# Kernel optimization log

Measured on AMD Instinct MI355X. Metric: run time of the kernel, lower is better.

Reference implementation:

```python
import jax, jax.numpy as jnp
import numpy as np

N, K, D, V = 20000, 16, 256, 64  # nodes, neighbors, embed_dim, edge vocab


def setup_inputs() -> dict:
    key = jax.random.key(0)
    ks = jax.random.split(key, 16)
    s = 1.0 / np.sqrt(2 * D)  # Linear(512 -> 256) init scale
    return {
        "node_reps": jax.random.normal(ks[0], (1, N, D), jnp.float32),
        "in_indices": jax.random.randint(ks[1], (1, N, K), 0, N, jnp.int32),
        "in_edges": jax.random.randint(ks[2], (1, N, K), 0, V, jnp.int32),
        "in_mask": jax.random.uniform(ks[3], (1, N, K), jnp.float32),
        "out_indices": jax.random.randint(ks[4], (1, N, K), 0, N, jnp.int32),
        "out_edges": jax.random.randint(ks[5], (1, N, K), 0, V, jnp.int32),
        "out_mask": jax.random.uniform(ks[6], (1, N, K), jnp.float32),
        "edge_emb_1": jax.random.normal(ks[7], (V, D), jnp.float32),
        "W_1": jax.random.uniform(ks[8], (2 * D, D), jnp.float32, -s, s),
        "b_1": jnp.zeros((D,), jnp.float32),
        "edge_emb_2": jax.random.normal(ks[9], (V, D), jnp.float32),
        "W_2": jax.random.uniform(ks[10], (2 * D, D), jnp.float32, -s, s),
        "b_2": jnp.zeros((D,), jnp.float32),
        "edge_emb_3": jax.random.normal(ks[11], (V, D), jnp.float32),
        "W_3": jax.random.uniform(ks[12], (2 * D, D), jnp.float32, -s, s),
        "b_3": jnp.zeros((D,), jnp.float32),
    }


def gcn_layer(node_reps, in_idx, in_edg, in_msk, out_idx, out_edg, out_msk,
              edge_emb, W, b):
    # node_reps: [1, N, D]; dropout is identity in eval mode.
    nodes = node_reps[0]  # [N, D]; batch_size == 1 as in the original repo

    def agg(idx, edg, msk):
        nbr = nodes[idx]          # gather: [1, N, K, D]
        erep = edge_emb[edg]      # embedding lookup: [1, N, K, D]
        reps = jnp.concatenate([nbr, erep], axis=3) * msk[..., None]
        return reps.sum(axis=2)   # masked sum over neighbors: [1, N, 2D]

    in_reps = agg(in_idx, in_edg, in_msk)
    out_reps = agg(out_idx, out_edg, out_msk)
    in_nodes = in_reps[0] @ W + b    # [N, D]
    out_nodes = out_reps[0] @ W + b  # [N, D]
    return node_reps + out_nodes + in_nodes  # broadcast -> [1, N, D]


def reference(node_reps, in_indices, in_edges, in_mask,
              out_indices, out_edges, out_mask,
              edge_emb_1, W_1, b_1, edge_emb_2, W_2, b_2, edge_emb_3, W_3, b_3):
    nbrs = (in_indices, in_edges, in_mask, out_indices, out_edges, out_mask)
    hidden = gcn_layer(node_reps, *nbrs, edge_emb_1, W_1, b_1)  # gc1
    mu = gcn_layer(hidden, *nbrs, edge_emb_2, W_2, b_2)          # gc2
    logvar = gcn_layer(hidden, *nbrs, edge_emb_3, W_3, b_3)      # gc3

    mu_t = jnp.tanh(mu[0])        # [N, D]
    lv_t = jnp.tanh(logvar[0])    # [N, D]
    n_nodes = mu_t.shape[0]
    kld = (-0.5 / n_nodes) * jnp.mean(
        jnp.sum(1.0 + 2.0 * lv_t - mu_t ** 2 - jnp.exp(lv_t) ** 2, axis=1))
    return hidden, kld
```

## Files before the change

### kernel.cpp

```cpp
#include <hip/hip_runtime.h>
#include <math.h>

#define NN 20000
#define KK 16
#define DD 256
#define VV 64
#define NT1 16
#define NT23 32

typedef __attribute__((ext_vector_type(8))) __bf16 bf16x8;
typedef __attribute__((ext_vector_type(4))) float floatx4;
typedef __attribute__((ext_vector_type(2))) float floatx2;
typedef __attribute__((ext_vector_type(8))) unsigned short ushort8;

__device__ __forceinline__ float4 ld4(const float* p) { return *reinterpret_cast<const float4*>(p); }

__device__ __forceinline__ unsigned short f2bf(float f) {
    union { float f; unsigned u; } v; v.f = f;
    unsigned r = v.u + 0x7FFFu + ((v.u >> 16) & 1u);
    return (unsigned short)(r >> 16);
}
__device__ __forceinline__ float bf2f(unsigned short u) {
    union { unsigned u; float f; } v; v.u = ((unsigned)u) << 16;
    return v.f;
}
__device__ __forceinline__ unsigned char f2q(float f) {
    return (unsigned char)(__builtin_amdgcn_cvt_pk_fp8_f32(f, 0.f, 0u, false) & 0xFFu);
}
__device__ __forceinline__ float q2f(unsigned char q) {
    floatx2 r = __builtin_amdgcn_cvt_pk_f32_fp8((unsigned)q, false);
    return r.x;
}

__global__ __launch_bounds__(256) void ewk3(const float* __restrict__ e1, const float* __restrict__ W1,
                                            const float* __restrict__ e2, const float* __restrict__ W2,
                                            const float* __restrict__ e3, const float* __restrict__ W3,
                                            float* __restrict__ EW) {
    int layer = blockIdx.y;
    const float* emb = layer == 0 ? e1 : (layer == 1 ? e2 : e3);
    const float* W   = layer == 0 ? W1 : (layer == 1 ? W2 : W3);
    int v = blockIdx.x, d = threadIdx.x;
    float acc = 0.f;
    #pragma unroll 8
    for (int j = 0; j < 256; ++j)
        acc += emb[v * DD + j] * W[(size_t)(256 + j) * DD + d];
    EW[(size_t)layer * VV * DD + v * DD + d] = acc;
}

__global__ __launch_bounds__(256) void packU2(const float* __restrict__ W1, const float* __restrict__ EW1,
                                              const float* __restrict__ W2, const float* __restrict__ EW2,
                                              const float* __restrict__ W3, const float* __restrict__ EW3,
                                              unsigned short* __restrict__ U1, unsigned short* __restrict__ U23) {
    int blk = blockIdx.x;
    int NT; unsigned short* U; const float *Wa, *EWa, *Wb, *EWb; int g;
    if (blk < 40) { NT = NT1;  U = U1;  Wa = W1; EWa = EW1; Wb = W1; EWb = EW1; g = blk * 256 + threadIdx.x; }
    else          { NT = NT23; U = U23; Wa = W2; EWa = EW2; Wb = W3; EWb = EW3; g = (blk - 40) * 256 + threadIdx.x; }
    int lane = g & 63, ntk = g >> 6;
    int nt = ntk % NT, kt = ntk / NT;
    if (kt >= 10) return;
    int n = nt * 16 + (lane & 15);
    int kbase = kt * 32 + (lane >> 4) * 8;
    const float* W = Wa; const float* EW = EWa;
    if (n >= 256) { W = Wb; EW = EWb; n -= 256; }
    unsigned short o8[8];
    #pragma unroll
    for (int j = 0; j < 8; ++j) {
        int k = kbase + j;
        float v = (k < 256) ? W[(size_t)k * DD + n] : EW[(size_t)(k - 256) * DD + n];
        o8[j] = f2bf(v);
    }
    *reinterpret_cast<uint4*>(&U[(size_t)g * 8]) = *reinterpret_cast<uint4*>(o8);
}

__global__ __launch_bounds__(256) void prep(const int* __restrict__ ie, const float* __restrict__ im,
                                            const int* __restrict__ oe, const float* __restrict__ om,
                                            const float* __restrict__ x,
                                            unsigned short* __restrict__ Sb, unsigned short* __restrict__ xh) {
    int w = threadIdx.x >> 6, lane = threadIdx.x & 63;
    int n = blockIdx.x * 4 + w;
    int e = 0; float m = 0.f;
    if (lane < 16)      { e = ie[n * KK + lane];      m = im[n * KK + lane]; }
    else if (lane < 32) { e = oe[n * KK + lane - 16]; m = om[n * KK + lane - 16]; }
    float h = 0.f;
    #pragma unroll
    for (int j = 0; j < 32; ++j) {
        int ev = __shfl(e, j);
        float mv = __shfl(m, j);
        if (ev == lane) h += mv;
    }
    Sb[(size_t)n * 320 + 256 + lane] = f2bf(h);
    if (xh) {
        size_t base = (size_t)blockIdx.x * 1024 + threadIdx.x * 4;
        float4 v = ld4(x + base);
        ushort4 o; o.x = f2bf(v.x); o.y = f2bf(v.y); o.z = f2bf(v.z); o.w = f2bf(v.w);
        *reinterpret_cast<ushort4*>(xh + base) = o;
    }
}

__global__ __launch_bounds__(256) void aggh(const unsigned short* __restrict__ src, const int* __restrict__ ii,
                                            const float* __restrict__ im, const int* __restrict__ oi,
                                            const float* __restrict__ om, unsigned short* __restrict__ Sb) {
    int w = threadIdx.x >> 6, lane = threadIdx.x & 63;
    int n = blockIdx.x * 4 + w;
    __shared__ int sidx[4][32];
    __shared__ float smsk[4][32];
    if (lane < 16) {
        sidx[w][lane] = ii[n * KK + lane]; sidx[w][lane + 16] = oi[n * KK + lane];
        smsk[w][lane] = im[n * KK + lane]; smsk[w][lane + 16] = om[n * KK + lane];
    }
    __syncthreads();
    int half = lane >> 5, c = (lane & 31) * 8;
    float acc[8] = {0.f, 0.f, 0.f, 0.f, 0.f, 0.f, 0.f, 0.f};
    #pragma unroll
    for (int j = 0; j < 16; ++j) {
        int j2 = j * 2 + half;
        int idx = sidx[w][j2];
        float m = smsk[w][j2];
        ushort8 u = *reinterpret_cast<const ushort8*>(src + (size_t)idx * DD + c);
        #pragma unroll
        for (int z = 0; z < 8; ++z) acc[z] += m * bf2f(u[z]);
    }
    #pragma unroll
    for (int z = 0; z < 8; ++z) acc[z] += __shfl_xor(acc[z], 32);
    if (half == 0) {
        unsigned short o8[8];
        #pragma unroll
        for (int z = 0; z < 8; ++z) o8[z] = f2bf(acc[z]);
        *reinterpret_cast<uint4*>(&Sb[(size_t)n * 320 + c]) = *reinterpret_cast<uint4*>(o8);
    }
}

__global__ __launch_bounds__(256) void aggq(const unsigned char* __restrict__ src, const int* __restrict__ ii,
                                            const float* __restrict__ im, const int* __restrict__ oi,
                                            const float* __restrict__ om, unsigned short* __restrict__ Sb) {
    int w = threadIdx.x >> 6, lane = threadIdx.x & 63;
    int n = blockIdx.x * 4 + w;
    __shared__ int sidx[4][32];
    __shared__ float smsk[4][32];
    if (lane < 16) {
        sidx[w][lane] = ii[n * KK + lane]; sidx[w][lane + 16] = oi[n * KK + lane];
        smsk[w][lane] = im[n * KK + lane]; smsk[w][lane + 16] = om[n * KK + lane];
    }
    __syncthreads();
    int g = lane >> 4, cl = lane & 15;
    float acc[16];
    #pragma unroll
    for (int z = 0; z < 16; ++z) acc[z] = 0.f;
    #pragma unroll
    for (int j = 0; j < 8; ++j) {
        int r = g * 8 + j;
        int idx = sidx[w][r];
        float m = smsk[w][r];
        uint4 u = *reinterpret_cast<const uint4*>(src + (size_t)idx * DD + cl * 16);
        unsigned dw[4] = {u.x, u.y, u.z, u.w};
        #pragma unroll
        for (int d = 0; d < 4; ++d) {
            floatx2 f01 = __builtin_amdgcn_cvt_pk_f32_fp8(dw[d], false);
            floatx2 f23 = __builtin_amdgcn_cvt_pk_f32_fp8(dw[d], true);
            acc[d * 4 + 0] += m * f01.x; acc[d * 4 + 1] += m * f01.y;
            acc[d * 4 + 2] += m * f23.x; acc[d * 4 + 3] += m * f23.y;
        }
    }
    #pragma unroll
    for (int z = 0; z < 16; ++z) {
        acc[z] += __shfl_xor(acc[z], 16);
        acc[z] += __shfl_xor(acc[z], 32);
    }
    if (g == 0) {
        unsigned short o16[16];
        #pragma unroll
        for (int z = 0; z < 16; ++z) o16[z] = f2bf(acc[z]);
        uint4* dst = reinterpret_cast<uint4*>(&Sb[(size_t)n * 320 + cl * 16]);
        dst[0] = reinterpret_cast<uint4*>(o16)[0];
        dst[1] = reinterpret_cast<uint4*>(o16)[1];
    }
}

__global__ __launch_bounds__(256) void aggf(const float* __restrict__ src, const int* __restrict__ ii,
                                            const float* __restrict__ im, const int* __restrict__ oi,
                                            const float* __restrict__ om, unsigned short* __restrict__ Sb) {
    int w = threadIdx.x >> 6, lane = threadIdx.x & 63;
    int n = blockIdx.x * 4 + w;
    __shared__ int sidx[4][32];
    __shared__ float smsk[4][32];
    if (lane < 16) {
        sidx[w][lane] = ii[n * KK + lane]; sidx[w][lane + 16] = oi[n * KK + lane];
        smsk[w][lane] = im[n * KK + lane]; smsk[w][lane + 16] = om[n * KK + lane];
    }
    __syncthreads();
    int c = lane * 4;
    float4 s = make_float4(0.f, 0.f, 0.f, 0.f);
    #pragma unroll 4
    for (int j = 0; j < 32; ++j) {
        float4 xr = ld4(src + (size_t)sidx[w][j] * DD + c);
        float m = smsk[w][j];
        s.x += m * xr.x; s.y += m * xr.y; s.z += m * xr.z; s.w += m * xr.w;
    }
    ushort4 o; o.x = f2bf(s.x); o.y = f2bf(s.y); o.z = f2bf(s.z); o.w = f2bf(s.w);
    *reinterpret_cast<ushort4*>(&Sb[(size_t)n * 320 + c]) = o;
}

__global__ __launch_bounds__(256) void mm1(const unsigned short* __restrict__ Sb, const unsigned short* __restrict__ U,
                                           const float* __restrict__ x, const float* __restrict__ b,
                                           float* __restrict__ out, unsigned char* __restrict__ h8) {
    __shared__ unsigned short sA[16 * 336];
    int n0 = blockIdx.x * 16;
    for (int c = threadIdx.x; c < 640; c += 256) {
        int row = c / 40, k8 = c % 40;
        *reinterpret_cast<uint4*>(&sA[row * 336 + k8 * 8]) =
            *reinterpret_cast<const uint4*>(&Sb[(size_t)(n0 + row) * 320 + k8 * 8]);
    }
    __syncthreads();
    int lane = threadIdx.x & 63, w = threadIdx.x >> 6;
    int lr = lane & 15, quad = lane >> 4;
    float xp[4][4], bb[4];
    #pragma unroll
    for (int t = 0; t < 4; ++t) {
        int col = (w * 4 + t) * 16 + lr;
        bb[t] = 2.f * b[col];
        #pragma unroll
        for (int r = 0; r < 4; ++r)
            xp[t][r] = x[(size_t)(n0 + quad * 4 + r) * DD + col];
    }
    floatx4 z = {0.f, 0.f, 0.f, 0.f};
    floatx4 acc[4] = {z, z, z, z};
    for (int kt = 0; kt < 10; ++kt) {
        bf16x8 a = *reinterpret_cast<const bf16x8*>(&sA[lr * 336 + kt * 32 + quad * 8]);
        #pragma unroll
        for (int t = 0; t < 4; ++t) {
            bf16x8 bf = *reinterpret_cast<const bf16x8*>(&U[(size_t)((kt * NT1 + w * 4 + t) * 64 + lane) * 8]);
            acc[t] = __builtin_amdgcn_mfma_f32_16x16x32_bf16(a, bf, acc[t], 0, 0, 0);
        }
    }
    #pragma unroll
    for (int t = 0; t < 4; ++t) {
        int col = (w * 4 + t) * 16 + lr;
        #pragma unroll
        for (int r = 0; r < 4; ++r) {
            size_t o = (size_t)(n0 + quad * 4 + r) * DD + col;
            float v = xp[t][r] + bb[t] + acc[t][r];
            out[o] = v;
            if (h8) h8[o] = f2q(v);
        }
    }
}

__global__ __launch_bounds__(256) void mm23(const unsigned short* __restrict__ Sb, const unsigned short* __restrict__ U,
                                            const unsigned char* __restrict__ h8, const float* __restrict__ hf,
                                            const float* __restrict__ b2, const float* __restrict__ b3,
                                            float* __restrict__ partials) {
    __shared__ unsigned short sA[16 * 336];
    __shared__ float red[4];
    int n0 = blockIdx.x * 16, pass = blockIdx.y;
    for (int c = threadIdx.x; c < 640; c += 256) {
        int row = c / 40, k8 = c % 40;
        *reinterpret_cast<uint4*>(&sA[row * 336 + k8 * 8]) =
            *reinterpret_cast<const uint4*>(&Sb[(size_t)(n0 + row) * 320 + k8 * 8]);
    }
    __syncthreads();
    int lane = threadIdx.x & 63, w = threadIdx.x >> 6;
    int lr = lane & 15, quad = lane >> 4;
    const float* b = pass ? b3 : b2;
    float hp[4][4], bb[4];
    #pragma unroll
    for (int t = 0; t < 4; ++t) {
        int col = (w * 4 + t) * 16 + lr;
        bb[t] = 2.f * b[col];
        #pragma unroll
        for (int r = 0; r < 4; ++r) {
            size_t o = (size_t)(n0 + quad * 4 + r) * DD + col;
            hp[t][r] = h8 ? q2f(h8[o]) : hf[o];
        }
    }
    floatx4 z = {0.f, 0.f, 0.f, 0.f};
    floatx4 acc[4] = {z, z, z, z};
    for (int kt = 0; kt < 10; ++kt) {
        bf16x8 a = *reinterpret_cast<const bf16x8*>(&sA[lr * 336 + kt * 32 + quad * 8]);
        #pragma unroll
        for (int t = 0; t < 4; ++t) {
            int nt = pass * 16 + w * 4 + t;
            bf16x8 bf = *reinterpret_cast<const bf16x8*>(&U[(size_t)((kt * NT23 + nt) * 64 + lane) * 8]);
            acc[t] = __builtin_amdgcn_mfma_f32_16x16x32_bf16(a, bf, acc[t], 0, 0, 0);
        }
    }
    float kacc = 0.f;
    #pragma unroll
    for (int t = 0; t < 4; ++t) {
        #pragma unroll
        for (int r = 0; r < 4; ++r) {
            float v = hp[t][r] + bb[t] + acc[t][r];
            float e = __expf(2.f * v);
            float tt = 1.f - 2.f * __builtin_amdgcn_rcpf(e + 1.f);
            kacc += (pass == 0) ? (1.f - tt * tt) : (2.f * tt - __expf(2.f * tt));
        }
    }
    #pragma unroll
    for (int off = 32; off > 0; off >>= 1) kacc += __shfl_xor(kacc, off);
    if (lane == 0) red[w] = kacc;
    __syncthreads();
    if (threadIdx.x == 0)
        partials[pass * 1250 + blockIdx.x] = red[0] + red[1] + red[2] + red[3];
}

__global__ __launch_bounds__(256) void kred(const float* __restrict__ partials, int np,
                                            float* __restrict__ out) {
    __shared__ double red[256];
    double l = 0.0;
    for (int i = threadIdx.x; i < np; i += 256) l += (double)partials[i];
    red[threadIdx.x] = l;
    __syncthreads();
    for (int s = 128; s > 0; s >>= 1) {
        if (threadIdx.x < s) red[threadIdx.x] += red[threadIdx.x + s];
        __syncthreads();
    }
    if (threadIdx.x == 0)
        out[0] = (float)(red[0] * (-0.5 / ((double)NN * (double)NN)));
}

extern "C" void kernel_launch(void* const* d_in, const int* in_sizes, int n_in,
                              void* d_out, int out_size, void* d_ws, size_t ws_size,
                              hipStream_t stream) {
    const float* x  = (const float*)d_in[0];
    const int*   ii = (const int*)d_in[1];
    const int*   ie = (const int*)d_in[2];
    const float* im = (const float*)d_in[3];
    const int*   oi = (const int*)d_in[4];
    const int*   oe = (const int*)d_in[5];
    const float* om = (const float*)d_in[6];
    const float* e1 = (const float*)d_in[7];
    const float* W1 = (const float*)d_in[8];
    const float* b1 = (const float*)d_in[9];
    const float* e2 = (const float*)d_in[10];
    const float* W2 = (const float*)d_in[11];
    const float* b2 = (const float*)d_in[12];
    const float* e3 = (const float*)d_in[13];
    const float* W3 = (const float*)d_in[14];
    const float* b3 = (const float*)d_in[15];
    float* out = (float*)d_out;

    char* ws = (char*)d_ws;
    float*          EW    = (float*)(ws);
    unsigned short* U1    = (unsigned short*)(ws + 196608);
    unsigned short* U23   = (unsigned short*)(ws + 360448);
    float*          parts = (float*)(ws + 688128);
    unsigned short* Sb    = (unsigned short*)(ws + 698128);
    unsigned short* xh    = (unsigned short*)(ws + 13498128);
    unsigned char*  h8    = (unsigned char*)(ws + 23738128);
    int useBf = ws_size >= (size_t)28858128;

    ewk3  <<<dim3(VV, 3), 256, 0, stream>>>(e1, W1, e2, W2, e3, W3, EW);
    packU2<<<120, 256, 0, stream>>>(W1, EW, W2, EW + VV * DD, W3, EW + 2 * VV * DD, U1, U23);
    prep  <<<NN / 4, 256, 0, stream>>>(ie, im, oe, om, x, Sb, useBf ? xh : (unsigned short*)nullptr);
    if (useBf) {
        aggh<<<NN / 4, 256, 0, stream>>>(xh, ii, im, oi, om, Sb);
        mm1 <<<NN / 16, 256, 0, stream>>>(Sb, U1, x, b1, out, h8);
        aggq<<<NN / 4, 256, 0, stream>>>(h8, ii, im, oi, om, Sb);
        mm23<<<dim3(NN / 16, 2), 256, 0, stream>>>(Sb, U23, h8, (const float*)nullptr, b2, b3, parts);
    } else {
        aggf<<<NN / 4, 256, 0, stream>>>(x, ii, im, oi, om, Sb);
        mm1 <<<NN / 16, 256, 0, stream>>>(Sb, U1, x, b1, out, (unsigned char*)nullptr);
        aggf<<<NN / 4, 256, 0, stream>>>(out, ii, im, oi, om, Sb);
        mm23<<<dim3(NN / 16, 2), 256, 0, stream>>>(Sb, U23, (const unsigned char*)nullptr, out, b2, b3, parts);
    }
    kred<<<1, 256, 0, stream>>>(parts, 2500, out + (size_t)NN * DD);
}
```

Measured before the change: 230.7 us.

## Fuse neighbor aggregation into GEMM kernels and merge mu/logvar passes

Aggregation kernels (aggh, aggq) are folded into the matmul kernels, so each block gathers its 16 rows directly into shared memory instead of writing and rereading an Sb staging buffer. The mu and logvar passes are merged into one block that computes both outputs from the same A tile, which halves the gather and A loads for layers 2 and 3. The residual x in layer 1 is now read from the bf16 copy, and the fp32 fallback path is removed. The trade-off is lower parallelism per block (16 rows each, 1250 blocks), higher register pressure from dual accumulators, and slightly lower precision in the residual.

```diff
diff --git a/kernel.cpp b/kernel.cpp
--- a/kernel.cpp
+++ b/kernel.cpp
@@ -6,7 +6,6 @@
 #define DD 256
 #define VV 64
 #define NT1 16
-#define NT23 32
 
 typedef __attribute__((ext_vector_type(8))) __bf16 bf16x8;
 typedef __attribute__((ext_vector_type(4))) float floatx4;
@@ -30,6 +29,10 @@
 __device__ __forceinline__ float q2f(unsigned char q) {
     floatx2 r = __builtin_amdgcn_cvt_pk_f32_fp8((unsigned)q, false);
     return r.x;
+}
+__device__ __forceinline__ float ftanh(float v) {
+    float e = __expf(2.f * v);
+    return 1.f - 2.f * __builtin_amdgcn_rcpf(e + 1.f);
 }
 
 __global__ __launch_bounds__(256) void ewk3(const float* __restrict__ e1, const float* __restrict__ W1,
@@ -53,8 +56,8 @@
                                               unsigned short* __restrict__ U1, unsigned short* __restrict__ U23) {
     int blk = blockIdx.x;
     int NT; unsigned short* U; const float *Wa, *EWa, *Wb, *EWb; int g;
-    if (blk < 40) { NT = NT1;  U = U1;  Wa = W1; EWa = EW1; Wb = W1; EWb = EW1; g = blk * 256 + threadIdx.x; }
-    else          { NT = NT23; U = U23; Wa = W2; EWa = EW2; Wb = W3; EWb = EW3; g = (blk - 40) * 256 + threadIdx.x; }
+    if (blk < 40) { NT = 16; U = U1;  Wa = W1; EWa = EW1; Wb = W1; EWb = EW1; g = blk * 256 + threadIdx.x; }
+    else          { NT = 32; U = U23; Wa = W2; EWa = EW2; Wb = W3; EWb = EW3; g = (blk - 40) * 256 + threadIdx.x; }
     int lane = g & 63, ntk = g >> 6;
     int nt = ntk % NT, kt = ntk / NT;
     if (kt >= 10) return;
@@ -75,7 +78,7 @@
 __global__ __launch_bounds__(256) void prep(const int* __restrict__ ie, const float* __restrict__ im,
                                             const int* __restrict__ oe, const float* __restrict__ om,
                                             const float* __restrict__ x,
-                                            unsigned short* __restrict__ Sb, unsigned short* __restrict__ xh) {
+                                            unsigned short* __restrict__ Hc, unsigned short* __restrict__ xh) {
     int w = threadIdx.x >> 6, lane = threadIdx.x & 63;
     int n = blockIdx.x * 4 + w;
     int e = 0; float m = 0.f;
@@ -88,130 +91,60 @@
         float mv = __shfl(m, j);
         if (ev == lane) h += mv;
     }
-    Sb[(size_t)n * 320 + 256 + lane] = f2bf(h);
-    if (xh) {
-        size_t base = (size_t)blockIdx.x * 1024 + threadIdx.x * 4;
-        float4 v = ld4(x + base);
-        ushort4 o; o.x = f2bf(v.x); o.y = f2bf(v.y); o.z = f2bf(v.z); o.w = f2bf(v.w);
-        *reinterpret_cast<ushort4*>(xh + base) = o;
-    }
-}
-
-__global__ __launch_bounds__(256) void aggh(const unsigned short* __restrict__ src, const int* __restrict__ ii,
-                                            const float* __restrict__ im, const int* __restrict__ oi,
-                                            const float* __restrict__ om, unsigned short* __restrict__ Sb) {
-    int w = threadIdx.x >> 6, lane = threadIdx.x & 63;
-    int n = blockIdx.x * 4 + w;
-    __shared__ int sidx[4][32];
-    __shared__ float smsk[4][32];
-    if (lane < 16) {
-        sidx[w][lane] = ii[n * KK + lane]; sidx[w][lane + 16] = oi[n * KK + lane];
-        smsk[w][lane] = im[n * KK + lane]; smsk[w][lane + 16] = om[n * KK + lane];
-    }
-    __syncthreads();
+    Hc[(size_t)n * 64 + lane] = f2bf(h);
+    size_t base = (size_t)blockIdx.x * 1024 + threadIdx.x * 4;
+    float4 v = ld4(x + base);
+    ushort4 o; o.x = f2bf(v.x); o.y = f2bf(v.y); o.z = f2bf(v.z); o.w = f2bf(v.w);
+    *reinterpret_cast<ushort4*>(xh + base) = o;
+}
+
+__global__ __launch_bounds__(256) void fmm1(const unsigned short* __restrict__ xh, const unsigned short* __restrict__ Hc,
+                                            const int* __restrict__ ii, const float* __restrict__ im,
+                                            const int* __restrict__ oi, const float* __restrict__ om,
+                                            const unsigned short* __restrict__ U, const float* __restrict__ b,
+                                            float* __restrict__ out, unsigned char* __restrict__ h8) {
+    __shared__ unsigned short sA[16 * 336];
+    __shared__ int sidx[16][32];
+    __shared__ float smsk[16][32];
+    int n0 = blockIdx.x * 16;
+    int tid = threadIdx.x;
+    for (int q = tid; q < 512; q += 256) {
+        int r = q >> 5, j = q & 31;
+        int n = n0 + r;
+        sidx[r][j] = (j < 16) ? ii[n * KK + j] : oi[n * KK + j - 16];
+        smsk[r][j] = (j < 16) ? im[n * KK + j] : om[n * KK + j - 16];
+    }
+    if (tid < 128) {
+        int r = tid >> 3, k8 = tid & 7;
+        *reinterpret_cast<uint4*>(&sA[r * 336 + 256 + k8 * 8]) =
+            *reinterpret_cast<const uint4*>(&Hc[(size_t)(n0 + r) * 64 + k8 * 8]);
+    }
+    __syncthreads();
+    int lane = tid & 63, w = tid >> 6;
     int half = lane >> 5, c = (lane & 31) * 8;
-    float acc[8] = {0.f, 0.f, 0.f, 0.f, 0.f, 0.f, 0.f, 0.f};
-    #pragma unroll
-    for (int j = 0; j < 16; ++j) {
-        int j2 = j * 2 + half;
-        int idx = sidx[w][j2];
-        float m = smsk[w][j2];
-        ushort8 u = *reinterpret_cast<const ushort8*>(src + (size_t)idx * DD + c);
-        #pragma unroll
-        for (int z = 0; z < 8; ++z) acc[z] += m * bf2f(u[z]);
-    }
-    #pragma unroll
-    for (int z = 0; z < 8; ++z) acc[z] += __shfl_xor(acc[z], 32);
-    if (half == 0) {
-        unsigned short o8[8];
-        #pragma unroll
-        for (int z = 0; z < 8; ++z) o8[z] = f2bf(acc[z]);
-        *reinterpret_cast<uint4*>(&Sb[(size_t)n * 320 + c]) = *reinterpret_cast<uint4*>(o8);
-    }
-}
-
-__global__ __launch_bounds__(256) void aggq(const unsigned char* __restrict__ src, const int* __restrict__ ii,
-                                            const float* __restrict__ im, const int* __restrict__ oi,
-                                            const float* __restrict__ om, unsigned short* __restrict__ Sb) {
-    int w = threadIdx.x >> 6, lane = threadIdx.x & 63;
-    int n = blockIdx.x * 4 + w;
-    __shared__ int sidx[4][32];
-    __shared__ float smsk[4][32];
-    if (lane < 16) {
-        sidx[w][lane] = ii[n * KK + lane]; sidx[w][lane + 16] = oi[n * KK + lane];
-        smsk[w][lane] = im[n * KK + lane]; smsk[w][lane + 16] = om[n * KK + lane];
-    }
-    __syncthreads();
-    int g = lane >> 4, cl = lane & 15;
-    float acc[16];
-    #pragma unroll
-    for (int z = 0; z < 16; ++z) acc[z] = 0.f;
-    #pragma unroll
-    for (int j = 0; j < 8; ++j) {
-        int r = g * 8 + j;
-        int idx = sidx[w][r];
-        float m = smsk[w][r];
-        uint4 u = *reinterpret_cast<const uint4*>(src + (size_t)idx * DD + cl * 16);
-        unsigned dw[4] = {u.x, u.y, u.z, u.w};
-        #pragma unroll
-        for (int d = 0; d < 4; ++d) {
-            floatx2 f01 = __builtin_amdgcn_cvt_pk_f32_fp8(dw[d], false);
-            floatx2 f23 = __builtin_amdgcn_cvt_pk_f32_fp8(dw[d], true);
-            acc[d * 4 + 0] += m * f01.x; acc[d * 4 + 1] += m * f01.y;
-            acc[d * 4 + 2] += m * f23.x; acc[d * 4 + 3] += m * f23.y;
-        }
-    }
-    #pragma unroll
-    for (int z = 0; z < 16; ++z) {
-        acc[z] += __shfl_xor(acc[z], 16);
-        acc[z] += __shfl_xor(acc[z], 32);
-    }
-    if (g == 0) {
-        unsigned short o16[16];
-        #pragma unroll
-        for (int z = 0; z < 16; ++z) o16[z] = f2bf(acc[z]);
-        uint4* dst = reinterpret_cast<uint4*>(&Sb[(size_t)n * 320 + cl * 16]);
-        dst[0] = reinterpret_cast<uint4*>(o16)[0];
-        dst[1] = reinterpret_cast<uint4*>(o16)[1];
-    }
-}
-
-__global__ __launch_bounds__(256) void aggf(const float* __restrict__ src, const int* __restrict__ ii,
-                                            const float* __restrict__ im, const int* __restrict__ oi,
-                                            const float* __restrict__ om, unsigned short* __restrict__ Sb) {
-    int w = threadIdx.x >> 6, lane = threadIdx.x & 63;
-    int n = blockIdx.x * 4 + w;
-    __shared__ int sidx[4][32];
-    __shared__ float smsk[4][32];
-    if (lane < 16) {
-        sidx[w][lane] = ii[n * KK + lane]; sidx[w][lane + 16] = oi[n * KK + lane];
-        smsk[w][lane] = im[n * KK + lane]; smsk[w][lane + 16] = om[n * KK + lane];
-    }
-    __syncthreads();
-    int c = lane * 4;
-    float4 s = make_float4(0.f, 0.f, 0.f, 0.f);
-    #pragma unroll 4
-    for (int j = 0; j < 32; ++j) {
-        float4 xr = ld4(src + (size_t)sidx[w][j] * DD + c);
-        float m = smsk[w][j];
-        s.x += m * xr.x; s.y += m * xr.y; s.z += m * xr.z; s.w += m * xr.w;
-    }
-    ushort4 o; o.x = f2bf(s.x); o.y = f2bf(s.y); o.z = f2bf(s.z); o.w = f2bf(s.w);
-    *reinterpret_cast<ushort4*>(&Sb[(size_t)n * 320 + c]) = o;
-}
-
-__global__ __launch_bounds__(256) void mm1(const unsigned short* __restrict__ Sb, const unsigned short* __restrict__ U,
-                                           const float* __restrict__ x, const float* __restrict__ b,
-                                           float* __restrict__ out, unsigned char* __restrict__ h8) {
-    __shared__ unsigned short sA[16 * 336];
-    int n0 = blockIdx.x * 16;
-    for (int c = threadIdx.x; c < 640; c += 256) {
-        int row = c / 40, k8 = c % 40;
-        *reinterpret_cast<uint4*>(&sA[row * 336 + k8 * 8]) =
-            *reinterpret_cast<const uint4*>(&Sb[(size_t)(n0 + row) * 320 + k8 * 8]);
-    }
-    __syncthreads();
-    int lane = threadIdx.x & 63, w = threadIdx.x >> 6;
+    #pragma unroll
+    for (int rr = 0; rr < 4; ++rr) {
+        int row = w * 4 + rr;
+        float acc[8] = {0.f, 0.f, 0.f, 0.f, 0.f, 0.f, 0.f, 0.f};
+        #pragma unroll
+        for (int j = 0; j < 16; ++j) {
+            int j2 = j * 2 + half;
+            int idx = sidx[row][j2];
+            float m = smsk[row][j2];
+            ushort8 u = *reinterpret_cast<const ushort8*>(xh + (size_t)idx * DD + c);
+            #pragma unroll
+            for (int z = 0; z < 8; ++z) acc[z] += m * bf2f(u[z]);
+        }
+        #pragma unroll
+        for (int z = 0; z < 8; ++z) acc[z] += __shfl_xor(acc[z], 32);
+        if (half == 0) {
+            unsigned short o8[8];
+            #pragma unroll
+            for (int z = 0; z < 8; ++z) o8[z] = f2bf(acc[z]);
+            *reinterpret_cast<uint4*>(&sA[row * 336 + c]) = *reinterpret_cast<uint4*>(o8);
+        }
+    }
+    __syncthreads();
     int lr = lane & 15, quad = lane >> 4;
     float xp[4][4], bb[4];
     #pragma unroll
@@ -220,7 +153,7 @@
         bb[t] = 2.f * b[col];
         #pragma unroll
         for (int r = 0; r < 4; ++r)
-            xp[t][r] = x[(size_t)(n0 + quad * 4 + r) * DD + col];
+            xp[t][r] = bf2f(xh[(size_t)(n0 + quad * 4 + r) * DD + col]);
     }
     floatx4 z = {0.f, 0.f, 0.f, 0.f};
     floatx4 acc[4] = {z, z, z, z};
@@ -240,47 +173,95 @@
             size_t o = (size_t)(n0 + quad * 4 + r) * DD + col;
             float v = xp[t][r] + bb[t] + acc[t][r];
             out[o] = v;
-            if (h8) h8[o] = f2q(v);
-        }
-    }
-}
-
-__global__ __launch_bounds__(256) void mm23(const unsigned short* __restrict__ Sb, const unsigned short* __restrict__ U,
-                                            const unsigned char* __restrict__ h8, const float* __restrict__ hf,
-                                            const float* __restrict__ b2, const float* __restrict__ b3,
-                                            float* __restrict__ partials) {
+            h8[o] = f2q(v);
+        }
+    }
+}
+
+__global__ __launch_bounds__(256) void fmm23(const unsigned char* __restrict__ h8, const unsigned short* __restrict__ Hc,
+                                             const int* __restrict__ ii, const float* __restrict__ im,
+                                             const int* __restrict__ oi, const float* __restrict__ om,
+                                             const unsigned short* __restrict__ U, const float* __restrict__ b2,
+                                             const float* __restrict__ b3, float* __restrict__ partials) {
     __shared__ unsigned short sA[16 * 336];
+    __shared__ int sidx[16][32];
+    __shared__ float smsk[16][32];
     __shared__ float red[4];
-    int n0 = blockIdx.x * 16, pass = blockIdx.y;
-    for (int c = threadIdx.x; c < 640; c += 256) {
-        int row = c / 40, k8 = c % 40;
-        *reinterpret_cast<uint4*>(&sA[row * 336 + k8 * 8]) =
-            *reinterpret_cast<const uint4*>(&Sb[(size_t)(n0 + row) * 320 + k8 * 8]);
-    }
-    __syncthreads();
-    int lane = threadIdx.x & 63, w = threadIdx.x >> 6;
+    int n0 = blockIdx.x * 16;
+    int tid = threadIdx.x;
+    for (int q = tid; q < 512; q += 256) {
+        int r = q >> 5, j = q & 31;
+        int n = n0 + r;
+        sidx[r][j] = (j < 16) ? ii[n * KK + j] : oi[n * KK + j - 16];
+        smsk[r][j] = (j < 16) ? im[n * KK + j] : om[n * KK + j - 16];
+    }
+    if (tid < 128) {
+        int r = tid >> 3, k8 = tid & 7;
+        *reinterpret_cast<uint4*>(&sA[r * 336 + 256 + k8 * 8]) =
+            *reinterpret_cast<const uint4*>(&Hc[(size_t)(n0 + r) * 64 + k8 * 8]);
+    }
+    __syncthreads();
+    int lane = tid & 63, w = tid >> 6;
+    int g = lane >> 4, cl = lane & 15;
+    #pragma unroll
+    for (int rr = 0; rr < 4; ++rr) {
+        int row = w * 4 + rr;
+        float acc[16];
+        #pragma unroll
+        for (int z = 0; z < 16; ++z) acc[z] = 0.f;
+        #pragma unroll
+        for (int j = 0; j < 8; ++j) {
+            int r = g * 8 + j;
+            int idx = sidx[row][r];
+            float m = smsk[row][r];
+            uint4 u = *reinterpret_cast<const uint4*>(h8 + (size_t)idx * DD + cl * 16);
+            unsigned dw[4] = {u.x, u.y, u.z, u.w};
+            #pragma unroll
+            for (int d = 0; d < 4; ++d) {
+                floatx2 f01 = __builtin_amdgcn_cvt_pk_f32_fp8(dw[d], false);
+                floatx2 f23 = __builtin_amdgcn_cvt_pk_f32_fp8(dw[d], true);
+                acc[d * 4 + 0] += m * f01.x; acc[d * 4 + 1] += m * f01.y;
+                acc[d * 4 + 2] += m * f23.x; acc[d * 4 + 3] += m * f23.y;
+            }
+        }
+        #pragma unroll
+        for (int z = 0; z < 16; ++z) {
+            acc[z] += __shfl_xor(acc[z], 16);
+            acc[z] += __shfl_xor(acc[z], 32);
+        }
+        if (g == 0) {
+            unsigned short o16[16];
+            #pragma unroll
+            for (int z = 0; z < 16; ++z) o16[z] = f2bf(acc[z]);
+            uint4* dst = reinterpret_cast<uint4*>(&sA[row * 336 + cl * 16]);
+            dst[0] = reinterpret_cast<uint4*>(o16)[0];
+            dst[1] = reinterpret_cast<uint4*>(o16)[1];
+        }
+    }
+    __syncthreads();
     int lr = lane & 15, quad = lane >> 4;
-    const float* b = pass ? b3 : b2;
-    float hp[4][4], bb[4];
+    float hp[4][4], bm[4], bl[4];
     #pragma unroll
     for (int t = 0; t < 4; ++t) {
         int col = (w * 4 + t) * 16 + lr;
-        bb[t] = 2.f * b[col];
-        #pragma unroll
-        for (int r = 0; r < 4; ++r) {
-            size_t o = (size_t)(n0 + quad * 4 + r) * DD + col;
-            hp[t][r] = h8 ? q2f(h8[o]) : hf[o];
-        }
+        bm[t] = 2.f * b2[col];
+        bl[t] = 2.f * b3[col];
+        #pragma unroll
+        for (int r = 0; r < 4; ++r)
+            hp[t][r] = q2f(h8[(size_t)(n0 + quad * 4 + r) * DD + col]);
     }
     floatx4 z = {0.f, 0.f, 0.f, 0.f};
-    floatx4 acc[4] = {z, z, z, z};
+    floatx4 am[4] = {z, z, z, z};
+    floatx4 al[4] = {z, z, z, z};
     for (int kt = 0; kt < 10; ++kt) {
         bf16x8 a = *reinterpret_cast<const bf16x8*>(&sA[lr * 336 + kt * 32 + quad * 8]);
         #pragma unroll
         for (int t = 0; t < 4; ++t) {
-            int nt = pass * 16 + w * 4 + t;
-            bf16x8 bf = *reinterpret_cast<const bf16x8*>(&U[(size_t)((kt * NT23 + nt) * 64 + lane) * 8]);
-            acc[t] = __builtin_amdgcn_mfma_f32_16x16x32_bf16(a, bf, acc[t], 0, 0, 0);
+            int nt = w * 4 + t;
+            bf16x8 bmu = *reinterpret_cast<const bf16x8*>(&U[(size_t)((kt * 32 + nt) * 64 + lane) * 8]);
+            bf16x8 blv = *reinterpret_cast<const bf16x8*>(&U[(size_t)((kt * 32 + 16 + nt) * 64 + lane) * 8]);
+            am[t] = __builtin_amdgcn_mfma_f32_16x16x32_bf16(a, bmu, am[t], 0, 0, 0);
+            al[t] = __builtin_amdgcn_mfma_f32_16x16x32_bf16(a, blv, al[t], 0, 0, 0);
         }
     }
     float kacc = 0.f;
@@ -288,18 +269,18 @@
     for (int t = 0; t < 4; ++t) {
         #pragma unroll
         for (int r = 0; r < 4; ++r) {
-            float v = hp[t][r] + bb[t] + acc[t][r];
-            float e = __expf(2.f * v);
-            float tt = 1.f - 2.f * __builtin_amdgcn_rcpf(e + 1.f);
-            kacc += (pass == 0) ? (1.f - tt * tt) : (2.f * tt - __expf(2.f * tt));
+            float h = hp[t][r];
+            float tm = ftanh(h + bm[t] + am[t][r]);
+            float tl = ftanh(h + bl[t] + al[t][r]);
+            kacc += (1.f - tm * tm) + (2.f * tl - __expf(2.f * tl));
         }
     }
     #pragma unroll
     for (int off = 32; off > 0; off >>= 1) kacc += __shfl_xor(kacc, off);
     if (lane == 0) red[w] = kacc;
     __syncthreads();
-    if (threadIdx.x == 0)
-        partials[pass * 1250 + blockIdx.x] = red[0] + red[1] + red[2] + red[3];
+    if (tid == 0)
+        partials[blockIdx.x] = red[0] + red[1] + red[2] + red[3];
 }
 
 __global__ __launch_bounds__(256) void kred(const float* __restrict__ partials, int np,
@@ -343,24 +324,14 @@
     unsigned short* U1    = (unsigned short*)(ws + 196608);
     unsigned short* U23   = (unsigned short*)(ws + 360448);
     float*          parts = (float*)(ws + 688128);
-    unsigned short* Sb    = (unsigned short*)(ws + 698128);
-    unsigned short* xh    = (unsigned short*)(ws + 13498128);
-    unsigned char*  h8    = (unsigned char*)(ws + 23738128);
-    int useBf = ws_size >= (size_t)28858128;
+    unsigned short* Hc    = (unsigned short*)(ws + 696128);
+    unsigned short* xh    = (unsigned short*)(ws + 3256128);
+    unsigned char*  h8    = (unsigned char*)(ws + 13496128);
 
     ewk3  <<<dim3(VV, 3), 256, 0, stream>>>(e1, W1, e2, W2, e3, W3, EW);
     packU2<<<120, 256, 0, stream>>>(W1, EW, W2, EW + VV * DD, W3, EW + 2 * VV * DD, U1, U23);
-    prep  <<<NN / 4, 256, 0, stream>>>(ie, im, oe, om, x, Sb, useBf ? xh : (unsigned short*)nullptr);
-    if (useBf) {
-        aggh<<<NN / 4, 256, 0, stream>>>(xh, ii, im, oi, om, Sb);
-        mm1 <<<NN / 16, 256, 0, stream>>>(Sb, U1, x, b1, out, h8);
-        aggq<<<NN / 4, 256, 0, stream>>>(h8, ii, im, oi, om, Sb);
-        mm23<<<dim3(NN / 16, 2), 256, 0, stream>>>(Sb, U23, h8, (const float*)nullptr, b2, b3, parts);
-    } else {
-        aggf<<<NN / 4, 256, 0, stream>>>(x, ii, im, oi, om, Sb);
-        mm1 <<<NN / 16, 256, 0, stream>>>(Sb, U1, x, b1, out, (unsigned char*)nullptr);
-        aggf<<<NN / 4, 256, 0, stream>>>(out, ii, im, oi, om, Sb);
-        mm23<<<dim3(NN / 16, 2), 256, 0, stream>>>(Sb, U23, (const unsigned char*)nullptr, out, b2, b3, parts);
-    }
-    kred<<<1, 256, 0, stream>>>(parts, 2500, out + (size_t)NN * DD);
-}
+    prep  <<<NN / 4, 256, 0, stream>>>(ie, im, oe, om, x, Hc, xh);
+    fmm1  <<<NN / 16, 256, 0, stream>>>(xh, Hc, ii, im, oi, om, U1, b1, out, h8);
+    fmm23 <<<NN / 16, 256, 0, stream>>>(h8, Hc, ii, im, oi, om, U23, b2, b3, parts);
+    kred  <<<1, 256, 0, stream>>>(parts, NN / 16, out + (size_t)NN * DD);
+}
```

Result: faster. 223.8 us (-3.0%).
